# Kernel tuning notes

Hardware: AMD Instinct MI355X
Metric: run time of the kernel (lower is better)

## Reference

```python
import jax, jax.numpy as jnp
import numpy as np

PATCH = 9  # patch_size (kernel_size=1, stride=1, padding=0, dilation_patch=1)


def setup_inputs() -> dict:
    key = jax.random.key(0)
    k1, k2 = jax.random.split(key)
    B, C, H, W = 4, 256, 128, 128
    return {
        "input1": jax.random.normal(k1, (B, C, H, W), dtype=jnp.float32),
        "input2": jax.random.normal(k2, (B, C, H, W), dtype=jnp.float32),
    }


def _correlation(input1, input2, patch=PATCH):
    # Faithful to torch _correlation_patch_based fast path:
    # corr[b, dy*P+dx, h, w] = sum_c input1[b,c,h,w] * input2_pad[b,c,h+dy,w+dx]
    # where input2 is zero-padded by P//2 (matches F.unfold padding=P//2).
    B, C, H, W = input1.shape
    pad = patch // 2
    i2p = jnp.pad(input2, ((0, 0), (0, 0), (pad, pad), (pad, pad)))
    # displacement offsets in unfold order: ky-major, kx-minor
    offs = jnp.stack(
        jnp.meshgrid(jnp.arange(patch), jnp.arange(patch), indexing="ij"), axis=-1
    ).reshape(-1, 2)  # (P*P, 2)

    def body(carry, off):
        # shifted window of input2, same (B,C,H,W) footprint (no unfold blowup)
        win = jax.lax.dynamic_slice(i2p, (0, 0, off[0], off[1]), (B, C, H, W))
        return carry, jnp.einsum("bchw,bchw->bhw", input1, win)

    _, corr = jax.lax.scan(body, None, offs)  # (P*P, B, H, W)
    return jnp.transpose(corr, (1, 0, 2, 3))  # (B, P*P, H, W)


def reference(input1, input2):
    return _correlation(input1, input2)
```

## Files before the change

### kernel.cpp

```cpp
#include <hip/hip_runtime.h>

#define BB   4
#define CC   256
#define HH   128
#define WW   128
#define PAD  4
#define KOUT 81

#define TH   8
#define SW   16
#define KC   32
#define NCHUNK (CC / KC)
#define AK   40

typedef _Float16 half8 __attribute__((ext_vector_type(8)));
typedef float    f32x4 __attribute__((ext_vector_type(4)));

__global__ __launch_bounds__(512, 4)
void corr_mfma2(const float* __restrict__ i1,
                const float* __restrict__ i2,
                float* __restrict__ out)
{
    __shared__ _Float16 Ald[128 * AK];
    __shared__ _Float16 Bld[512 * AK];

    const int t    = threadIdx.x;
    const int wave = t >> 6;
    const int lane = t & 63;
    const int l15  = lane & 15;
    const int quad = lane >> 4;

    const int b  = blockIdx.z;
    const int h0 = blockIdx.y * TH;
    const int w0 = blockIdx.x * SW;

    const size_t strideC = (size_t)HH * WW;
    const float* i1b = i1 + (size_t)b * CC * strideC;
    const float* i2b = i2 + (size_t)b * CC * strideC;

    bool valid;
    const float* gptr;
    _Float16* ldst;
    if (t < 384) {
        const int sq  = t % 24;
        const int sr  = t / 24;
        const int col = w0 - PAD + sq;
        const int row = h0 - PAD + sr;
        valid = (col >= 0) && (col < WW) && (row >= 0) && (row < HH);
        const int crow = valid ? row : 0;
        const int ccol = valid ? col : 0;
        gptr = i2b + (size_t)crow * WW + ccol;
        ldst = &Bld[(sr * 32 + sq) * AK];
    } else {
        const int i  = t - 384;
        const int sm = i & 15;
        const int sr = i >> 4;
        valid = true;
        gptr = i1b + (size_t)(h0 + sr) * WW + (w0 + sm);
        ldst = &Ald[(sr * 16 + sm) * AK];
    }

    f32x4 acc[9][2];
#pragma unroll
    for (int dy = 0; dy < 9; ++dy) {
        acc[dy][0] = (f32x4){0.f, 0.f, 0.f, 0.f};
        acc[dy][1] = (f32x4){0.f, 0.f, 0.f, 0.f};
    }

    float v[KC];

#pragma unroll
    for (int j = 0; j < KC; ++j)
        v[j] = valid ? gptr[(size_t)j * strideC] : 0.f;
#pragma unroll
    for (int u = 0; u < 4; ++u) {
        half8 hv;
#pragma unroll
        for (int k = 0; k < 8; ++k) hv[k] = (_Float16)v[8 * u + k];
        *(half8*)&ldst[8 * u] = hv;
    }
    __syncthreads();

#pragma unroll 1
    for (int ch = 0; ch < NCHUNK; ++ch) {
        if (ch + 1 < NCHUNK) {
            const float* g = gptr + (size_t)(ch + 1) * KC * strideC;
#pragma unroll
            for (int j = 0; j < KC; ++j)
                v[j] = valid ? g[(size_t)j * strideC] : 0.f;
        }

        {
            const half8 a = *(const half8*)&Ald[(wave * 16 + l15) * AK + quad * 8];
#pragma unroll
            for (int dy = 0; dy < 9; ++dy) {
                const int r = wave + dy;
                const half8 b0 = *(const half8*)&Bld[(r * 32 + l15) * AK + quad * 8];
                acc[dy][0] = __builtin_amdgcn_mfma_f32_16x16x32_f16(a, b0, acc[dy][0], 0, 0, 0);
                const half8 b1 = *(const half8*)&Bld[(r * 32 + 16 + l15) * AK + quad * 8];
                acc[dy][1] = __builtin_amdgcn_mfma_f32_16x16x32_f16(a, b1, acc[dy][1], 0, 0, 0);
            }
        }

        if (ch + 1 < NCHUNK) {
            __syncthreads();
#pragma unroll
            for (int u = 0; u < 4; ++u) {
                half8 hv;
#pragma unroll
                for (int k = 0; k < 8; ++k) hv[k] = (_Float16)v[8 * u + k];
                *(half8*)&ldst[8 * u] = hv;
            }
            __syncthreads();
        }
    }

    const int h = h0 + wave;
#pragma unroll
    for (int dy = 0; dy < 9; ++dy) {
#pragma unroll
        for (int tt = 0; tt < 2; ++tt) {
#pragma unroll
            for (int reg = 0; reg < 4; ++reg) {
                const int p  = quad * 4 + reg;
                const int dx = l15 + 16 * tt - p;
                if (dx >= 0 && dx <= 8) {
                    out[(((size_t)b * KOUT + (dy * 9 + dx)) * HH + h) * WW + (w0 + p)] =
                        acc[dy][tt][reg];
                }
            }
        }
    }
}

extern "C" void kernel_launch(void* const* d_in, const int* in_sizes, int n_in,
                              void* d_out, int out_size, void* d_ws, size_t ws_size,
                              hipStream_t stream)
{
    (void)in_sizes; (void)n_in; (void)d_ws; (void)ws_size; (void)out_size;
    const float* i1 = (const float*)d_in[0];
    const float* i2 = (const float*)d_in[1];
    float* out = (float*)d_out;

    dim3 grid(WW / SW, HH / TH, BB);
    dim3 block(512);
    corr_mfma2<<<grid, block, 0, stream>>>(i1, i2, out);
}
```

Before: 186.9 us.

## Load inputs as float4 along width, splitting channels across threads

Reworks the global-to-LDS staging so each thread loads four adjacent width positions as a float4 for eight channels, instead of 32 scalar channel loads for a single pixel. Channel groups are spread across four threads and transposed into the half-precision LDS layout, with invalid border groups writing zeros once. This cuts the number of global load instructions and widens each access, at the cost of a more complex thread-to-data mapping. It assumes that padding-boundary validity can be decided per 4-wide group, which holds because the tile offsets are multiples of 4.

```diff
diff --git a/kernel.cpp b/kernel.cpp
--- a/kernel.cpp
+++ b/kernel.cpp
@@ -17,7 +17,7 @@
 typedef float    f32x4 __attribute__((ext_vector_type(4)));
 
 __global__ __launch_bounds__(512, 4)
-void corr_mfma2(const float* __restrict__ i1,
+void corr_mfma3(const float* __restrict__ i1,
                 const float* __restrict__ i2,
                 float* __restrict__ out)
 {
@@ -39,25 +39,30 @@
     const float* i2b = i2 + (size_t)b * CC * strideC;
 
     bool valid;
-    const float* gptr;
-    _Float16* ldst;
+    const float* gp;
+    _Float16* ld0;
+
     if (t < 384) {
-        const int sq  = t % 24;
-        const int sr  = t / 24;
-        const int col = w0 - PAD + sq;
-        const int row = h0 - PAD + sr;
-        valid = (col >= 0) && (col < WW) && (row >= 0) && (row < HH);
-        const int crow = valid ? row : 0;
-        const int ccol = valid ? col : 0;
-        gptr = i2b + (size_t)crow * WW + ccol;
-        ldst = &Bld[(sr * 32 + sq) * AK];
+        const int g   = t % 6;
+        const int t6  = t / 6;
+        const int ch8 = t6 & 3;
+        const int sr  = t6 >> 2;
+        const int row  = h0 - PAD + sr;
+        const int col0 = w0 - PAD + 4 * g;
+        valid = (row >= 0) && (row < HH) && (col0 >= 0) && (col0 + 3 < WW);
+        gp  = i2b + (size_t)(valid ? row : 0) * WW + (valid ? col0 : 0)
+                  + (size_t)ch8 * 8 * strideC;
+        ld0 = &Bld[(sr * 32 + 4 * g) * AK + ch8 * 8];
     } else {
-        const int i  = t - 384;
-        const int sm = i & 15;
-        const int sr = i >> 4;
+        const int i   = t - 384;
+        const int g   = i & 3;
+        const int t4  = i >> 2;
+        const int ch8 = t4 & 3;
+        const int sr  = t4 >> 2;
         valid = true;
-        gptr = i1b + (size_t)(h0 + sr) * WW + (w0 + sm);
-        ldst = &Ald[(sr * 16 + sm) * AK];
+        gp  = i1b + (size_t)(h0 + sr) * WW + (w0 + 4 * g)
+                  + (size_t)ch8 * 8 * strideC;
+        ld0 = &Ald[(sr * 16 + 4 * g) * AK + ch8 * 8];
     }
 
     f32x4 acc[9][2];
@@ -67,27 +72,34 @@
         acc[dy][1] = (f32x4){0.f, 0.f, 0.f, 0.f};
     }
 
-    float v[KC];
+    f32x4 L[8];
 
+    if (valid) {
 #pragma unroll
-    for (int j = 0; j < KC; ++j)
-        v[j] = valid ? gptr[(size_t)j * strideC] : 0.f;
+        for (int j = 0; j < 8; ++j)
+            L[j] = *(const f32x4*)(gp + (size_t)j * strideC);
 #pragma unroll
-    for (int u = 0; u < 4; ++u) {
-        half8 hv;
+        for (int i = 0; i < 4; ++i) {
+            half8 hv;
 #pragma unroll
-        for (int k = 0; k < 8; ++k) hv[k] = (_Float16)v[8 * u + k];
-        *(half8*)&ldst[8 * u] = hv;
+            for (int k = 0; k < 8; ++k) hv[k] = (_Float16)L[k][i];
+            *(half8*)(ld0 + i * AK) = hv;
+        }
+    } else {
+        const half8 z = (half8){0, 0, 0, 0, 0, 0, 0, 0};
+#pragma unroll
+        for (int i = 0; i < 4; ++i)
+            *(half8*)(ld0 + i * AK) = z;
     }
     __syncthreads();
 
 #pragma unroll 1
     for (int ch = 0; ch < NCHUNK; ++ch) {
-        if (ch + 1 < NCHUNK) {
-            const float* g = gptr + (size_t)(ch + 1) * KC * strideC;
+        if (valid && (ch + 1 < NCHUNK)) {
+            const float* gnext = gp + (size_t)(ch + 1) * KC * strideC;
 #pragma unroll
-            for (int j = 0; j < KC; ++j)
-                v[j] = valid ? g[(size_t)j * strideC] : 0.f;
+            for (int j = 0; j < 8; ++j)
+                L[j] = *(const f32x4*)(gnext + (size_t)j * strideC);
         }
 
         {
@@ -104,12 +116,14 @@
 
         if (ch + 1 < NCHUNK) {
             __syncthreads();
+            if (valid) {
 #pragma unroll
-            for (int u = 0; u < 4; ++u) {
-                half8 hv;
+                for (int i = 0; i < 4; ++i) {
+                    half8 hv;
 #pragma unroll
-                for (int k = 0; k < 8; ++k) hv[k] = (_Float16)v[8 * u + k];
-                *(half8*)&ldst[8 * u] = hv;
+                    for (int k = 0; k < 8; ++k) hv[k] = (_Float16)L[k][i];
+                    *(half8*)(ld0 + i * AK) = hv;
+                }
             }
             __syncthreads();
         }
@@ -144,5 +158,5 @@
 
     dim3 grid(WW / SW, HH / TH, BB);
     dim3 block(512);
-    corr_mfma2<<<grid, block, 0, stream>>>(i1, i2, out);
+    corr_mfma3<<<grid, block, 0, stream>>>(i1, i2, out);
 }
```

New measurement: 182.3 us. -2.5%, faster.
